# Kernel optimization log

Hardware: AMD Instinct MI355X
Metric: run time of the kernel (lower is better)

Reference implementation:

```python
import jax, jax.numpy as jnp
import numpy as np
import math

N_HEADS = 16
N_POINTS = 4
EPS = 1e-6


def layer_norm(x, g, b):
    m = x.mean(-1, keepdims=True)
    v = ((x - m) ** 2).mean(-1, keepdims=True)
    return (x - m) / jnp.sqrt(v + EPS) * g + b


def ref_points(H, W, dtype):
    # matches CrossSelfAtt.get_reference_points for one square level -> (1, H*W, 1, 2) in (x, y)
    ys = (jnp.arange(H, dtype=dtype) + 0.5) / H
    xs = (jnp.arange(W, dtype=dtype) + 0.5) / W
    gy, gx = jnp.meshgrid(ys, xs, indexing='ij')
    return jnp.stack([gx.reshape(-1), gy.reshape(-1)], -1)[None, :, None, :]


def bilinear(v, H, W, loc):
    # v: (B, H*W, nH, Dh); loc: (B, Lq, nH, P, 2) normalized [0,1]; zero padding, align_corners=False
    B, _, nH, Dh = v.shape
    Lq, P = loc.shape[1], loc.shape[3]
    x = loc[..., 0] * W - 0.5
    y = loc[..., 1] * H - 0.5
    x0 = jnp.floor(x)
    y0 = jnp.floor(y)
    wx1 = x - x0
    wy1 = y - y0
    x0i = x0.astype(jnp.int32)
    y0i = y0.astype(jnp.int32)
    vt = v.transpose(0, 2, 1, 3)  # (B, nH, HW, Dh)

    def corner(xi, yi, w):
        valid = (xi >= 0) & (xi < W) & (yi >= 0) & (yi < H)
        idx = jnp.clip(yi, 0, H - 1) * W + jnp.clip(xi, 0, W - 1)  # (B, Lq, nH, P)
        idx_t = idx.transpose(0, 2, 1, 3).reshape(B, nH, Lq * P)
        g = jnp.take_along_axis(vt, idx_t[..., None], axis=2).reshape(B, nH, Lq, P, Dh)
        return g.transpose(0, 2, 1, 3, 4) * (w * valid)[..., None]

    return (corner(x0i, y0i, (1 - wx1) * (1 - wy1))
            + corner(x0i + 1, y0i, wx1 * (1 - wy1))
            + corner(x0i, y0i + 1, (1 - wx1) * wy1)
            + corner(x0i + 1, y0i + 1, wx1 * wy1))


def msda(query, value_in, shapes, ref, Wv, bv, Woff, boff, Wa, ba, Wo, bo):
    # standard Deformable-DETR MSDeformAttn forward
    B, Lq, D = query.shape
    nH, P, L = N_HEADS, N_POINTS, len(shapes)
    Dh = D // nH
    value = (value_in @ Wv + bv).reshape(B, -1, nH, Dh)
    off = (query @ Woff + boff).reshape(B, Lq, nH, L, P, 2)
    aw = jax.nn.softmax((query @ Wa + ba).reshape(B, Lq, nH, L * P), -1).reshape(B, Lq, nH, L, P)
    norm = jnp.asarray([[w_, h_] for (h_, w_) in shapes], dtype=query.dtype)  # (L, 2) = (W, H)
    loc = ref[:, :, None, :, None, :] + off / norm[None, None, None, :, None, :]
    out = jnp.zeros((B, Lq, nH, Dh), query.dtype)
    start = 0
    for l, (H_, W_) in enumerate(shapes):
        samp = bilinear(value[:, start:start + H_ * W_], H_, W_, loc[:, :, :, l])
        out = out + (samp * aw[:, :, :, l, :, None]).sum(3)
        start += H_ * W_
    return out.reshape(B, Lq, D) @ Wo + bo


def setup_inputs() -> dict:
    key = jax.random.key(0)
    B, Lq, Lf, D = 2, 4096, 4096, 768
    nH, P, L = N_HEADS, N_POINTS, 1
    ks = jax.random.split(key, 20)
    w = lambda k, s: jax.random.normal(k, s, jnp.float32) * 0.02
    return {
        'query': jax.random.normal(ks[0], (B, Lq, D), jnp.float32),
        'feat': jax.random.normal(ks[1], (B, Lf, D), jnp.float32),
        'spatial_shapes': jnp.array([[64, 64]], jnp.int32),
        'level_start_index': jnp.array([0], jnp.int32),
        'qn_W': w(ks[2], (D, D)), 'qn_b': jnp.zeros((D,)), 'qn_g': jnp.ones((D,)), 'qn_beta': jnp.zeros((D,)),
        'fn_W': w(ks[3], (D, D)), 'fn_b': jnp.zeros((D,)), 'fn_g': jnp.ones((D,)), 'fn_beta': jnp.zeros((D,)),
        'nm_g': jnp.ones((D,)), 'nm_beta': jnp.zeros((D,)),
        'gamma1': jax.random.normal(ks[4], (D,), jnp.float32) * 0.1,
        'c_Wv': w(ks[5], (D, D)), 'c_bv': jnp.zeros((D,)),
        'c_Woff': w(ks[6], (D, nH * L * P * 2)),
        'c_boff': jax.random.uniform(ks[7], (nH * L * P * 2,), jnp.float32, -3.0, 3.0),
        'c_Wa': w(ks[8], (D, nH * L * P)), 'c_ba': jnp.zeros((nH * L * P,)),
        'c_Wo': w(ks[9], (D, D)), 'c_bo': jnp.zeros((D,)),
        's_Wv': w(ks[10], (D, D)), 's_bv': jnp.zeros((D,)),
        's_Woff': w(ks[11], (D, nH * L * P * 2)),
        's_boff': jax.random.uniform(ks[12], (nH * L * P * 2,), jnp.float32, -3.0, 3.0),
        's_Wa': w(ks[13], (D, nH * L * P)), 's_ba': jnp.zeros((nH * L * P,)),
        's_Wo': w(ks[14], (D, D)), 's_bo': jnp.zeros((D,)),
    }


def reference(query, feat, spatial_shapes, level_start_index, qn_W, qn_b, qn_g, qn_beta, fn_W, fn_b, fn_g, fn_beta, nm_g, nm_beta, gamma1, c_Wv, c_bv, c_Woff, c_boff, c_Wa, c_ba, c_Wo, c_bo, s_Wv, s_bv, s_Woff, s_boff, s_Wa, s_ba, s_Wo, s_bo):
    shapes = [(int(h), int(w_)) for h, w_ in np.asarray(spatial_shapes)]
    qe = int(math.sqrt(query.shape[1]))
    ref = ref_points(qe, qe, query.dtype)  # (1, Lq, 1, 2)
    qn = layer_norm(query @ qn_W + qn_b, qn_g, qn_beta)
    fn = layer_norm(feat @ fn_W + fn_b, fn_g, fn_beta)
    attn = msda(qn, fn, shapes, ref, c_Wv, c_bv, c_Woff, c_boff, c_Wa, c_ba, c_Wo, c_bo)
    attn1 = layer_norm(attn, nm_g, nm_beta)
    attn2 = msda(attn1, attn1, [(qe, qe)], ref, s_Wv, s_bv, s_Woff, s_boff, s_Wa, s_ba, s_Wo, s_bo)
    # note: source uses gamma1 for BOTH terms (gamma2 is unused)
    return attn * gamma1 + attn2 * gamma1
```

## Files before the change

kernel.cpp:

```cpp
#include <hip/hip_runtime.h>
#include <hip/hip_bf16.h>
#include <math.h>

#define D_MODEL 768
#define NH 16
#define DH 48
#define NP 4
#define LQ 4096
#define BB 2
#define MTOT (BB * LQ)

typedef __attribute__((ext_vector_type(8))) _Float16 half8_t;
typedef __attribute__((ext_vector_type(4))) float floatx4;

__device__ __forceinline__ void load_lds16(const void* g, void* l) {
    __builtin_amdgcn_global_load_lds((const __attribute__((address_space(1))) void*)g,
                                     (__attribute__((address_space(3))) void*)l, 16, 0, 0);
}

template <int MODE>
__device__ __forceinline__ void gemm_body(
    const _Float16* __restrict__ A, const _Float16* __restrict__ Wt,
    const float* __restrict__ bias, void* __restrict__ Cv, int ldc,
    int tm, int tn,
    const float* __restrict__ attn, const float* __restrict__ gamma)
{
    constexpr int K = 768;
    constexpr int NT = K / 32;
    __shared__ _Float16 As[2][128 * 32];
    __shared__ _Float16 Bs[2][128 * 32];

    const int bm = tm * 128, bn = tn * 128;
    const int t = threadIdx.x;
    const int lane = t & 63;
    const int w = t >> 6;
    const int wm = (w >> 1) * 64, wn = (w & 1) * 64;

    floatx4 acc[4][4] = {};

    const int r0 = t >> 2;
    const int c8 = (t & 3) * 8;
    const size_t arow0 = (size_t)(bm + r0) * K + c8;
    const size_t arow1 = (size_t)(bm + 64 + r0) * K + c8;
    const size_t brow0 = (size_t)(bn + r0) * K + c8;
    const size_t brow1 = (size_t)(bn + 64 + r0) * K + c8;

    const int lrow = lane & 15;
    const int lk = (lane >> 4) * 8;

    load_lds16(A + arow0, &As[0][w * 512]);
    load_lds16(A + arow1, &As[0][2048 + w * 512]);
    load_lds16(Wt + brow0, &Bs[0][w * 512]);
    load_lds16(Wt + brow1, &Bs[0][2048 + w * 512]);
    __syncthreads();

    for (int ti = 0; ti < NT; ++ti) {
        const int cur = ti & 1;
        if (ti + 1 < NT) {
            const int kn = (ti + 1) * 32;
            const int nxt = cur ^ 1;
            load_lds16(A + arow0 + kn, &As[nxt][w * 512]);
            load_lds16(A + arow1 + kn, &As[nxt][2048 + w * 512]);
            load_lds16(Wt + brow0 + kn, &Bs[nxt][w * 512]);
            load_lds16(Wt + brow1 + kn, &Bs[nxt][2048 + w * 512]);
        }

        const _Float16* Ac = As[cur];
        const _Float16* Bc = Bs[cur];
        half8_t af[4], bf[4];
#pragma unroll
        for (int i = 0; i < 4; ++i) {
            af[i] = *(const half8_t*)&Ac[(wm + i * 16 + lrow) * 32 + lk];
            bf[i] = *(const half8_t*)&Bc[(wn + i * 16 + lrow) * 32 + lk];
        }
#pragma unroll
        for (int i = 0; i < 4; ++i)
#pragma unroll
            for (int j = 0; j < 4; ++j)
                acc[i][j] = __builtin_amdgcn_mfma_f32_16x16x32_f16(af[i], bf[j], acc[i][j], 0, 0, 0);

        if (ti + 1 < NT) __syncthreads();
    }

    const int rquad = (lane >> 4) * 4;
#pragma unroll
    for (int i = 0; i < 4; ++i) {
#pragma unroll
        for (int j = 0; j < 4; ++j) {
            const int col = bn + wn + j * 16 + lrow;
            const float bcol = bias[col];
#pragma unroll
            for (int r = 0; r < 4; ++r) {
                const size_t row = (size_t)(bm + wm + i * 16 + rquad + r);
                float v = acc[i][j][r] + bcol;
                if (MODE == 1) v = (attn[row * ldc + col] + v) * gamma[col];
                if (MODE == 2) ((_Float16*)Cv)[row * (size_t)ldc + col] = (_Float16)v;
                else           ((float*)Cv)[row * (size_t)ldc + col] = v;
            }
        }
    }
}

template <int MODE>
__global__ __launch_bounds__(256) void gemm_mfma(
    const _Float16* __restrict__ A, const _Float16* __restrict__ Wt,
    const float* __restrict__ bias, void* __restrict__ C,
    const float* __restrict__ attn, const float* __restrict__ gamma)
{
    const int bid = blockIdx.x;
    const int swz = (bid & 7) * 48 + (bid >> 3);
    gemm_body<MODE>(A, Wt, bias, C, 768, swz & 63, swz >> 6, attn, gamma);
}

template <int M0, int M1>
__global__ __launch_bounds__(256) void dual_gemm(
    const _Float16* __restrict__ A0, const _Float16* __restrict__ W0,
    const float* __restrict__ b0, void* __restrict__ C0, int ldc0, int cnt0,
    const _Float16* __restrict__ A1, const _Float16* __restrict__ W1,
    const float* __restrict__ b1, void* __restrict__ C1, int ldc1, int cnt1)
{
    int bid = blockIdx.x;
    if (bid < cnt0) {
        const int q = cnt0 >> 3;
        const int swz = (bid & 7) * q + (bid >> 3);
        gemm_body<M0>(A0, W0, b0, C0, ldc0, swz & 63, swz >> 6, nullptr, nullptr);
    } else {
        bid -= cnt0;
        const int q = cnt1 >> 3;
        const int swz = (bid & 7) * q + (bid >> 3);
        gemm_body<M1>(A1, W1, b1, C1, ldc1, swz & 63, swz >> 6, nullptr, nullptr);
    }
}

__device__ __forceinline__ void ln_wave_body(
    const float* __restrict__ X, _Float16* __restrict__ A,
    const float* __restrict__ g, const float* __restrict__ beta, int row)
{
    const int lane = threadIdx.x & 63;
    const float* x = X + (size_t)row * D_MODEL;
    float v[12];
    float s = 0.f, s2 = 0.f;
#pragma unroll
    for (int j = 0; j < 12; ++j) {
        v[j] = x[lane + 64 * j];
        s += v[j];
        s2 += v[j] * v[j];
    }
#pragma unroll
    for (int m = 1; m < 64; m <<= 1) {
        s += __shfl_xor(s, m);
        s2 += __shfl_xor(s2, m);
    }
    const float mean = s * (1.f / 768.f);
    const float var = s2 * (1.f / 768.f) - mean * mean;
    const float rstd = rsqrtf(var + 1e-6f);
    _Float16* arow = A + (size_t)row * D_MODEL;
#pragma unroll
    for (int j = 0; j < 12; ++j) {
        const int cc = lane + 64 * j;
        arow[cc] = (_Float16)((v[j] - mean) * rstd * g[cc] + beta[cc]);
    }
}

__global__ __launch_bounds__(256) void ln2_wave(
    const float* __restrict__ X0, _Float16* __restrict__ A0,
    const float* __restrict__ g0, const float* __restrict__ b0,
    const float* __restrict__ X1, _Float16* __restrict__ A1,
    const float* __restrict__ g1, const float* __restrict__ b1)
{
    const int r = blockIdx.x * 4 + (threadIdx.x >> 6);
    if (r < MTOT) ln_wave_body(X0, A0, g0, b0, r);
    else          ln_wave_body(X1, A1, g1, b1, r - MTOT);
}

__global__ __launch_bounds__(256) void ln_wave(
    const float* __restrict__ X, _Float16* __restrict__ A,
    const float* __restrict__ g, const float* __restrict__ beta)
{
    const int r = blockIdx.x * 4 + (threadIdx.x >> 6);
    ln_wave_body(X, A, g, beta, r);
}

__global__ __launch_bounds__(256) void convert_all(
    const float* __restrict__ query, _Float16* __restrict__ actA,
    const float* __restrict__ feat, _Float16* __restrict__ actB,
    const float* __restrict__ w0, const float* __restrict__ w1,
    const float* __restrict__ w2, const float* __restrict__ w3,
    const float* __restrict__ w4, const float* __restrict__ w5,
    _Float16* __restrict__ Wall,
    const float* __restrict__ Woff_c, const float* __restrict__ Wa_c,
    const float* __restrict__ boff_c, const float* __restrict__ ba_c,
    const float* __restrict__ Woff_s, const float* __restrict__ Wa_s,
    const float* __restrict__ boff_s, const float* __restrict__ ba_s,
    _Float16* __restrict__ Wc, _Float16* __restrict__ Ws,
    float* __restrict__ bias_c, float* __restrict__ bias_s)
{
    __shared__ float tile[32][33];
    const int bid = blockIdx.x;
    const int t = threadIdx.x;

    if (bid < 12288) {
        const int i = bid * 256 + t;
        const int sel = i / (MTOT * 192);
        const int r = i - sel * (MTOT * 192);
        const float* X = sel ? feat : query;
        _Float16* D = sel ? actB : actA;
        const int c4 = r * 4;
        const float4 v = *(const float4*)(X + (size_t)c4);
        _Float16 o[4] = {(_Float16)v.x, (_Float16)v.y, (_Float16)v.z, (_Float16)v.w};
        *(uint2*)(D + (size_t)c4) = *(uint2*)o;
    } else if (bid < 15744) {
        const int g = bid - 12288;
        const int wi = g / 576;
        const int gx = g - wi * 576;
        const float* W = (wi == 0) ? w0 : (wi == 1) ? w1 : (wi == 2) ? w2
                       : (wi == 3) ? w3 : (wi == 4) ? w4 : w5;
        _Float16* Wt = Wall + (size_t)wi * 768 * 768;
        const int tk0 = (gx / 24) * 32;
        const int tn0 = (gx % 24) * 32;
#pragma unroll
        for (int r = 0; r < 4; ++r) {
            const int row = r * 8 + (t >> 5);
            const int col = t & 31;
            tile[row][col] = W[(size_t)(tk0 + row) * 768 + tn0 + col];
        }
        __syncthreads();
        const int n = t >> 3;
        const int kq = (t & 7) * 4;
        _Float16* dst = Wt + (size_t)(tn0 + n) * 768 + tk0 + kq;
#pragma unroll
        for (int u = 0; u < 4; ++u) dst[u] = (_Float16)tile[kq + u][n];
    } else {
        const int i = (bid - 15744) * 256 + t;
        if (i >= 2 * 256 * 192) return;
        const int pair = i / (256 * 192);
        const int r = i - pair * (256 * 192);
        const int n = r / 192;
        const int k0 = (r - n * 192) * 4;
        const float* Woff = pair ? Woff_s : Woff_c;
        const float* Wa = pair ? Wa_s : Wa_c;
        _Float16* dst = pair ? Ws : Wc;
        _Float16* row = dst + (size_t)n * 768;
#pragma unroll
        for (int u = 0; u < 4; ++u) {
            const int k = k0 + u;
            float v = (n < 128) ? Woff[(size_t)k * 128 + n]
                    : (n < 192) ? Wa[(size_t)k * 64 + (n - 128)] : 0.f;
            row[k] = (_Float16)v;
        }
        if (k0 == 0) {
            const float* boff = pair ? boff_s : boff_c;
            const float* ba = pair ? ba_s : ba_c;
            float* bias = pair ? bias_s : bias_c;
            bias[n] = (n < 128) ? boff[n] : (n < 192) ? ba[n - 128] : 0.f;
        }
    }
}

__global__ __launch_bounds__(192) void sample_fused(
    const _Float16* __restrict__ value, const float* __restrict__ offc,
    _Float16* __restrict__ A)
{
    __shared__ float loc_s[32][8];
    __shared__ float aw_s[32][4];

    const int bid = blockIdx.x;
    const int swz = (bid & 7) * 512 + (bid >> 3);
    const int bq_base = swz * 2;
    const int t = threadIdx.x;

    if (t < 32) {
        const int bq = bq_base + (t >> 4);
        const int h = t & 15;
        const int q = bq & (LQ - 1);
        const float* orow = offc + (size_t)bq * 256 + h * 8;
        const float* arow = offc + (size_t)bq * 256 + 128 + h * 4;
        float a0 = arow[0], a1 = arow[1], a2 = arow[2], a3 = arow[3];
        float mx = fmaxf(fmaxf(a0, a1), fmaxf(a2, a3));
        float e0 = expf(a0 - mx), e1 = expf(a1 - mx), e2 = expf(a2 - mx), e3 = expf(a3 - mx);
        float r = 1.f / (e0 + e1 + e2 + e3);
        const float refx = ((q & 63) + 0.5f) * (1.f / 64.f);
        const float refy = ((q >> 6) + 0.5f) * (1.f / 64.f);
#pragma unroll
        for (int p = 0; p < 4; ++p) {
            loc_s[t][p * 2 + 0] = refx + orow[p * 2 + 0] * (1.f / 64.f);
            loc_s[t][p * 2 + 1] = refy + orow[p * 2 + 1] * (1.f / 64.f);
        }
        aw_s[t][0] = e0 * r; aw_s[t][1] = e1 * r;
        aw_s[t][2] = e2 * r; aw_s[t][3] = e3 * r;
    }
    __syncthreads();

    const int lbqh = t / 6;
    const int c = t - lbqh * 6;
    const int d0 = c * 8;
    const int bq = bq_base + (lbqh >> 4);
    const int h = lbqh & 15;
    const int b = bq >> 12;

    const _Float16* vbase = value + (size_t)b * LQ * D_MODEL + h * DH + d0;

    float acc[8] = {};
#pragma unroll
    for (int p = 0; p < 4; ++p) {
        const float x = loc_s[lbqh][p * 2 + 0] * 64.f - 0.5f;
        const float y = loc_s[lbqh][p * 2 + 1] * 64.f - 0.5f;
        const float xf = floorf(x), yf = floorf(y);
        const float wx1 = x - xf, wy1 = y - yf;
        const float wx0 = 1.f - wx1, wy0 = 1.f - wy1;
        const int x0 = (int)xf, y0 = (int)yf;
        const int x1 = x0 + 1, y1 = y0 + 1;
        const float wp = aw_s[lbqh][p];
        const bool vx0 = (x0 >= 0) && (x0 < 64);
        const bool vx1 = (x1 >= 0) && (x1 < 64);
        const bool vy0 = (y0 >= 0) && (y0 < 64);
        const bool vy1 = (y1 >= 0) && (y1 < 64);
        const float cw[4] = {wp * wx0 * wy0, wp * wx1 * wy0, wp * wx0 * wy1, wp * wx1 * wy1};
        const bool cv[4] = {vx0 && vy0, vx1 && vy0, vx0 && vy1, vx1 && vy1};
        const int cxy[4][2] = {{x0, y0}, {x1, y0}, {x0, y1}, {x1, y1}};
#pragma unroll
        for (int k = 0; k < 4; ++k) {
            if (cv[k]) {
                const half8_t g = *(const half8_t*)(vbase + (size_t)(cxy[k][1] * 64 + cxy[k][0]) * D_MODEL);
#pragma unroll
                for (int u = 0; u < 8; ++u) acc[u] += cw[k] * (float)g[u];
            }
        }
    }

    _Float16* arow = A + (size_t)bq * D_MODEL + h * DH + d0;
    _Float16 o[8];
#pragma unroll
    for (int u = 0; u < 8; ++u) o[u] = (_Float16)acc[u];
    *(uint4*)arow = *(uint4*)o;
}

extern "C" void kernel_launch(void* const* d_in, const int* in_sizes, int n_in,
                              void* d_out, int out_size, void* d_ws, size_t ws_size,
                              hipStream_t stream)
{
    const float* query   = (const float*)d_in[0];
    const float* feat    = (const float*)d_in[1];
    const float* qn_W    = (const float*)d_in[4];
    const float* qn_b    = (const float*)d_in[5];
    const float* qn_g    = (const float*)d_in[6];
    const float* qn_beta = (const float*)d_in[7];
    const float* fn_W    = (const float*)d_in[8];
    const float* fn_b    = (const float*)d_in[9];
    const float* fn_g    = (const float*)d_in[10];
    const float* fn_beta = (const float*)d_in[11];
    const float* nm_g    = (const float*)d_in[12];
    const float* nm_beta = (const float*)d_in[13];
    const float* gamma1  = (const float*)d_in[14];
    const float* c_Wv    = (const float*)d_in[15];
    const float* c_bv    = (const float*)d_in[16];
    const float* c_Woff  = (const float*)d_in[17];
    const float* c_boff  = (const float*)d_in[18];
    const float* c_Wa    = (const float*)d_in[19];
    const float* c_ba    = (const float*)d_in[20];
    const float* c_Wo    = (const float*)d_in[21];
    const float* c_bo    = (const float*)d_in[22];
    const float* s_Wv    = (const float*)d_in[23];
    const float* s_bv    = (const float*)d_in[24];
    const float* s_Woff  = (const float*)d_in[25];
    const float* s_boff  = (const float*)d_in[26];
    const float* s_Wa    = (const float*)d_in[27];
    const float* s_ba    = (const float*)d_in[28];
    const float* s_Wo    = (const float*)d_in[29];
    const float* s_bo    = (const float*)d_in[30];

    float* ws = (float*)d_ws;
    const size_t SZ = (size_t)MTOT * D_MODEL;
    float* buf0 = ws;
    float* buf1 = ws + SZ;
    _Float16* val16 = (_Float16*)(ws + 2 * SZ);
    float* buf3 = ws + 3 * SZ;
    _Float16* slotA = (_Float16*)(ws + 4 * SZ);
    _Float16* slotB = (_Float16*)(ws + 4 * SZ + SZ / 2);
    float* bias_c = ws + 5 * SZ;
    float* bias_s = bias_c + 256;
    _Float16* W6 = (_Float16*)(bias_s + 256);
    _Float16* W_qn  = W6 + (size_t)0 * 768 * 768;
    _Float16* W_fn  = W6 + (size_t)1 * 768 * 768;
    _Float16* W_cWv = W6 + (size_t)2 * 768 * 768;
    _Float16* W_cWo = W6 + (size_t)3 * 768 * 768;
    _Float16* W_sWv = W6 + (size_t)4 * 768 * 768;
    _Float16* W_sWo = W6 + (size_t)5 * 768 * 768;
    _Float16* Woffa_c = W6 + (size_t)6 * 768 * 768;
    _Float16* Woffa_s = Woffa_c + (size_t)256 * 768;
    float* offc = buf0;

    float* out = (float*)d_out;
    const dim3 blk(256);

    convert_all<<<16128, blk, 0, stream>>>(
        query, slotA, feat, slotB,
        qn_W, fn_W, c_Wv, c_Wo, s_Wv, s_Wo, W6,
        c_Woff, c_Wa, c_boff, c_ba, s_Woff, s_Wa, s_boff, s_ba,
        Woffa_c, Woffa_s, bias_c, bias_s);

    dual_gemm<0, 0><<<768, blk, 0, stream>>>(slotA, W_qn, qn_b, buf0, 768, 384,
                                             slotB, W_fn, fn_b, buf1, 768, 384);
    ln2_wave<<<2 * MTOT / 4, blk, 0, stream>>>(buf0, slotA, qn_g, qn_beta,
                                               buf1, slotB, fn_g, fn_beta);
    dual_gemm<2, 0><<<512, blk, 0, stream>>>(slotB, W_cWv, c_bv, val16, 768, 384,
                                             slotA, Woffa_c, bias_c, offc, 256, 128);
    sample_fused<<<4096, dim3(192), 0, stream>>>(val16, offc, slotB);
    gemm_mfma<0><<<384, blk, 0, stream>>>(slotB, W_cWo, c_bo, buf3, nullptr, nullptr);

    ln_wave<<<MTOT / 4, blk, 0, stream>>>(buf3, slotA, nm_g, nm_beta);
    dual_gemm<2, 0><<<512, blk, 0, stream>>>(slotA, W_sWv, s_bv, val16, 768, 384,
                                             slotA, Woffa_s, bias_s, offc, 256, 128);
    sample_fused<<<4096, dim3(192), 0, stream>>>(val16, offc, slotB);
    gemm_mfma<1><<<384, blk, 0, stream>>>(slotB, W_sWo, s_bo, out, buf3, gamma1);
}
```

Baseline: 354.8 us.

## Triple-buffer GEMM LDS pipeline and store intermediates as fp16

The GEMM main loop moves from double to triple buffering. Tiles are prefetched two steps ahead, and explicit vmcnt waits plus raw s_barrier replace __syncthreads. Separately, the pre-LayerNorm GEMM outputs and the cross-attention output are written and read as fp16 instead of fp32, which halves the traffic through those intermediate buffers. The changes add LDS pressure and hand-tuned wait counts, and fp16 storage of the attn residual loses precision. LayerNorm now runs in place on the fp16 buffers.

```diff
diff --git a/kernel.cpp b/kernel.cpp
--- a/kernel.cpp
+++ b/kernel.cpp
@@ -23,12 +23,12 @@
     const _Float16* __restrict__ A, const _Float16* __restrict__ Wt,
     const float* __restrict__ bias, void* __restrict__ Cv, int ldc,
     int tm, int tn,
-    const float* __restrict__ attn, const float* __restrict__ gamma)
+    const _Float16* __restrict__ attn, const float* __restrict__ gamma)
 {
     constexpr int K = 768;
     constexpr int NT = K / 32;
-    __shared__ _Float16 As[2][128 * 32];
-    __shared__ _Float16 Bs[2][128 * 32];
+    __shared__ _Float16 As[3][128 * 32];
+    __shared__ _Float16 Bs[3][128 * 32];
 
     const int bm = tm * 128, bn = tn * 128;
     const int t = threadIdx.x;
@@ -48,25 +48,32 @@
     const int lrow = lane & 15;
     const int lk = (lane >> 4) * 8;
 
-    load_lds16(A + arow0, &As[0][w * 512]);
-    load_lds16(A + arow1, &As[0][2048 + w * 512]);
-    load_lds16(Wt + brow0, &Bs[0][w * 512]);
-    load_lds16(Wt + brow1, &Bs[0][2048 + w * 512]);
-    __syncthreads();
+    auto STAGE = [&](int step) {
+        const int b3 = step % 3;
+        const size_t kn = (size_t)step * 32;
+        _Float16* asb = &As[b3][0];
+        _Float16* bsb = &Bs[b3][0];
+        load_lds16(A + arow0 + kn, asb + w * 512);
+        load_lds16(A + arow1 + kn, asb + 2048 + w * 512);
+        load_lds16(Wt + brow0 + kn, bsb + w * 512);
+        load_lds16(Wt + brow1 + kn, bsb + 2048 + w * 512);
+    };
+
+    STAGE(0);
+    STAGE(1);
 
     for (int ti = 0; ti < NT; ++ti) {
-        const int cur = ti & 1;
-        if (ti + 1 < NT) {
-            const int kn = (ti + 1) * 32;
-            const int nxt = cur ^ 1;
-            load_lds16(A + arow0 + kn, &As[nxt][w * 512]);
-            load_lds16(A + arow1 + kn, &As[nxt][2048 + w * 512]);
-            load_lds16(Wt + brow0 + kn, &Bs[nxt][w * 512]);
-            load_lds16(Wt + brow1 + kn, &Bs[nxt][2048 + w * 512]);
-        }
-
-        const _Float16* Ac = As[cur];
-        const _Float16* Bc = Bs[cur];
+        const int cur = ti % 3;
+        if (ti + 2 < NT) STAGE(ti + 2);
+
+        if (ti < NT - 2)       asm volatile("s_waitcnt vmcnt(8)" ::: "memory");
+        else if (ti == NT - 2) asm volatile("s_waitcnt vmcnt(4)" ::: "memory");
+        else                   asm volatile("s_waitcnt vmcnt(0)" ::: "memory");
+        __builtin_amdgcn_s_barrier();
+        __builtin_amdgcn_sched_barrier(0);
+
+        const _Float16* Ac = &As[cur][0];
+        const _Float16* Bc = &Bs[cur][0];
         half8_t af[4], bf[4];
 #pragma unroll
         for (int i = 0; i < 4; ++i) {
@@ -79,7 +86,8 @@
             for (int j = 0; j < 4; ++j)
                 acc[i][j] = __builtin_amdgcn_mfma_f32_16x16x32_f16(af[i], bf[j], acc[i][j], 0, 0, 0);
 
-        if (ti + 1 < NT) __syncthreads();
+        __builtin_amdgcn_sched_barrier(0);
+        __builtin_amdgcn_s_barrier();
     }
 
     const int rquad = (lane >> 4) * 4;
@@ -93,9 +101,14 @@
             for (int r = 0; r < 4; ++r) {
                 const size_t row = (size_t)(bm + wm + i * 16 + rquad + r);
                 float v = acc[i][j][r] + bcol;
-                if (MODE == 1) v = (attn[row * ldc + col] + v) * gamma[col];
-                if (MODE == 2) ((_Float16*)Cv)[row * (size_t)ldc + col] = (_Float16)v;
-                else           ((float*)Cv)[row * (size_t)ldc + col] = v;
+                if constexpr (MODE == 1) {
+                    v = ((float)attn[row * (size_t)ldc + col] + v) * gamma[col];
+                    ((float*)Cv)[row * (size_t)ldc + col] = v;
+                } else if constexpr (MODE == 2) {
+                    ((_Float16*)Cv)[row * (size_t)ldc + col] = (_Float16)v;
+                } else {
+                    ((float*)Cv)[row * (size_t)ldc + col] = v;
+                }
             }
         }
     }
@@ -105,7 +118,7 @@
 __global__ __launch_bounds__(256) void gemm_mfma(
     const _Float16* __restrict__ A, const _Float16* __restrict__ Wt,
     const float* __restrict__ bias, void* __restrict__ C,
-    const float* __restrict__ attn, const float* __restrict__ gamma)
+    const _Float16* __restrict__ attn, const float* __restrict__ gamma)
 {
     const int bid = blockIdx.x;
     const int swz = (bid & 7) * 48 + (bid >> 3);
@@ -133,16 +146,16 @@
 }
 
 __device__ __forceinline__ void ln_wave_body(
-    const float* __restrict__ X, _Float16* __restrict__ A,
+    const _Float16* __restrict__ X, _Float16* __restrict__ A,
     const float* __restrict__ g, const float* __restrict__ beta, int row)
 {
     const int lane = threadIdx.x & 63;
-    const float* x = X + (size_t)row * D_MODEL;
+    const _Float16* x = X + (size_t)row * D_MODEL;
     float v[12];
     float s = 0.f, s2 = 0.f;
 #pragma unroll
     for (int j = 0; j < 12; ++j) {
-        v[j] = x[lane + 64 * j];
+        v[j] = (float)x[lane + 64 * j];
         s += v[j];
         s2 += v[j] * v[j];
     }
@@ -163,9 +176,9 @@
 }
 
 __global__ __launch_bounds__(256) void ln2_wave(
-    const float* __restrict__ X0, _Float16* __restrict__ A0,
+    const _Float16* __restrict__ X0, _Float16* __restrict__ A0,
     const float* __restrict__ g0, const float* __restrict__ b0,
-    const float* __restrict__ X1, _Float16* __restrict__ A1,
+    const _Float16* __restrict__ X1, _Float16* __restrict__ A1,
     const float* __restrict__ g1, const float* __restrict__ b1)
 {
     const int r = blockIdx.x * 4 + (threadIdx.x >> 6);
@@ -174,7 +187,7 @@
 }
 
 __global__ __launch_bounds__(256) void ln_wave(
-    const float* __restrict__ X, _Float16* __restrict__ A,
+    const _Float16* __restrict__ X, _Float16* __restrict__ A,
     const float* __restrict__ g, const float* __restrict__ beta)
 {
     const int r = blockIdx.x * 4 + (threadIdx.x >> 6);
@@ -369,15 +382,14 @@
     const float* s_Wo    = (const float*)d_in[29];
     const float* s_bo    = (const float*)d_in[30];
 
-    float* ws = (float*)d_ws;
     const size_t SZ = (size_t)MTOT * D_MODEL;
-    float* buf0 = ws;
-    float* buf1 = ws + SZ;
-    _Float16* val16 = (_Float16*)(ws + 2 * SZ);
-    float* buf3 = ws + 3 * SZ;
-    _Float16* slotA = (_Float16*)(ws + 4 * SZ);
-    _Float16* slotB = (_Float16*)(ws + 4 * SZ + SZ / 2);
-    float* bias_c = ws + 5 * SZ;
+    _Float16* hA    = (_Float16*)d_ws;
+    _Float16* hB    = hA + SZ;
+    _Float16* hQ    = hB + SZ;
+    _Float16* hF    = hQ + SZ;
+    _Float16* val16 = hF + SZ;
+    float* offc   = (float*)(val16 + SZ);
+    float* bias_c = offc + (size_t)MTOT * 256;
     float* bias_s = bias_c + 256;
     _Float16* W6 = (_Float16*)(bias_s + 256);
     _Float16* W_qn  = W6 + (size_t)0 * 768 * 768;
@@ -388,29 +400,28 @@
     _Float16* W_sWo = W6 + (size_t)5 * 768 * 768;
     _Float16* Woffa_c = W6 + (size_t)6 * 768 * 768;
     _Float16* Woffa_s = Woffa_c + (size_t)256 * 768;
-    float* offc = buf0;
 
     float* out = (float*)d_out;
     const dim3 blk(256);
 
     convert_all<<<16128, blk, 0, stream>>>(
-        query, slotA, feat, slotB,
+        query, hA, feat, hB,
         qn_W, fn_W, c_Wv, c_Wo, s_Wv, s_Wo, W6,
         c_Woff, c_Wa, c_boff, c_ba, s_Woff, s_Wa, s_boff, s_ba,
         Woffa_c, Woffa_s, bias_c, bias_s);
 
-    dual_gemm<0, 0><<<768, blk, 0, stream>>>(slotA, W_qn, qn_b, buf0, 768, 384,
-                                             slotB, W_fn, fn_b, buf1, 768, 384);
-    ln2_wave<<<2 * MTOT / 4, blk, 0, stream>>>(buf0, slotA, qn_g, qn_beta,
-                                               buf1, slotB, fn_g, fn_beta);
-    dual_gemm<2, 0><<<512, blk, 0, stream>>>(slotB, W_cWv, c_bv, val16, 768, 384,
-                                             slotA, Woffa_c, bias_c, offc, 256, 128);
-    sample_fused<<<4096, dim3(192), 0, stream>>>(val16, offc, slotB);
-    gemm_mfma<0><<<384, blk, 0, stream>>>(slotB, W_cWo, c_bo, buf3, nullptr, nullptr);
-
-    ln_wave<<<MTOT / 4, blk, 0, stream>>>(buf3, slotA, nm_g, nm_beta);
-    dual_gemm<2, 0><<<512, blk, 0, stream>>>(slotA, W_sWv, s_bv, val16, 768, 384,
-                                             slotA, Woffa_s, bias_s, offc, 256, 128);
-    sample_fused<<<4096, dim3(192), 0, stream>>>(val16, offc, slotB);
-    gemm_mfma<1><<<384, blk, 0, stream>>>(slotB, W_sWo, s_bo, out, buf3, gamma1);
-}
+    dual_gemm<2, 2><<<768, blk, 0, stream>>>(hA, W_qn, qn_b, hQ, 768, 384,
+                                             hB, W_fn, fn_b, hF, 768, 384);
+    ln2_wave<<<2 * MTOT / 4, blk, 0, stream>>>(hQ, hQ, qn_g, qn_beta,
+                                               hF, hF, fn_g, fn_beta);
+    dual_gemm<2, 0><<<512, blk, 0, stream>>>(hF, W_cWv, c_bv, val16, 768, 384,
+                                             hQ, Woffa_c, bias_c, offc, 256, 128);
+    sample_fused<<<4096, dim3(192), 0, stream>>>(val16, offc, hB);
+    gemm_mfma<2><<<384, blk, 0, stream>>>(hB, W_cWo, c_bo, hA, nullptr, nullptr);
+
+    ln_wave<<<MTOT / 4, blk, 0, stream>>>(hA, hQ, nm_g, nm_beta);
+    dual_gemm<2, 0><<<512, blk, 0, stream>>>(hQ, W_sWv, s_bv, val16, 768, 384,
+                                             hQ, Woffa_s, bias_s, offc, 256, 128);
+    sample_fused<<<4096, dim3(192), 0, stream>>>(val16, offc, hB);
+    gemm_mfma<1><<<384, blk, 0, stream>>>(hB, W_sWo, s_bo, out, hA, gamma1);
+}
```

Measured after the change: 365.7 us. 1.03x slower.
